# Kernel optimization log

Hardware: AMD Instinct MI355X
Metric: run time of the kernel (lower is better)

## Reference

```python
import jax, jax.numpy as jnp
import numpy as np


def setup_inputs() -> dict:
    key = jax.random.key(0)
    k1, k2, k3, k4, k5 = jax.random.split(key, 5)
    B, N, T, O, G = 32, 256, 1024, 1024, 8
    x = jax.random.normal(k1, (B, N, T), dtype=jnp.float32)
    y = jax.random.uniform(k2, (B, G), dtype=jnp.float32)  # genre mixture weights
    weight = jax.random.normal(k3, (G, O, T), dtype=jnp.float32) * (1.0 / np.sqrt(T))
    mask = jax.random.uniform(k4, (O, T), dtype=jnp.float32)
    bias = jax.random.normal(k5, (O,), dtype=jnp.float32)
    return {"x": x, "y": y, "weight": weight, "mask": mask, "bias": bias}


def reference(x, y, weight, mask, bias):
    # mask the shared weight bank: [G,O,T] * [1,O,T]
    masked_w = weight * mask[None, :, :]
    # per-sample genre-mixed weights: [B,G] x [G,O,T] -> [B,O,T]
    w_bot = jnp.einsum('bg,got->bot', y, masked_w)
    # batched masked linear: [B,N,T] x [B,O,T] -> [B,N,O], plus bias
    return jnp.einsum('bnt,bot->bno', x, w_bot) + bias
```

## Files before the change

kernel.cpp:

```cpp
#include <hip/hip_runtime.h>
#include <hip/hip_bf16.h>
#include <stdint.h>


#define B_ 32
#define N_ 256
#define T_ 1024
#define O_ 1024
#define G_ 8

#define WSTRIDE ((size_t)(O_ * T_ + 2048))

#define BM 128
#define BN 128
#define BK 64
#define BUFSZ (BM * BK)

typedef __attribute__((__ext_vector_type__(8)))  __bf16 bf16x8;
typedef __attribute__((__ext_vector_type__(16))) float  f32x16;

__device__ __forceinline__ unsigned short f2bf(float f) {
    union { float f; uint32_t u; } v; v.f = f;
    uint32_t u = v.u;
    uint32_t r = (u + 0x7fffu + ((u >> 16) & 1u)) >> 16;
    return (unsigned short)r;
}

__device__ __forceinline__ uint4 pack8(const float* a) {
    uint4 r;
    r.x = (uint32_t)f2bf(a[0]) | ((uint32_t)f2bf(a[1]) << 16);
    r.y = (uint32_t)f2bf(a[2]) | ((uint32_t)f2bf(a[3]) << 16);
    r.z = (uint32_t)f2bf(a[4]) | ((uint32_t)f2bf(a[5]) << 16);
    r.w = (uint32_t)f2bf(a[6]) | ((uint32_t)f2bf(a[7]) << 16);
    return r;
}

#define MIXB 1024
#define CVTB 1024

__global__ __launch_bounds__(256) void prep_kernel(
    const float* __restrict__ w,
    const float* __restrict__ mask,
    const float* __restrict__ y,
    const float* __restrict__ x,
    unsigned short* __restrict__ Wb,
    unsigned short* __restrict__ xb)
{
    const int tid = threadIdx.x;
    if (blockIdx.x < MIXB) {
        const int idx = blockIdx.x * 256 + tid;
        const int o   = idx >> 8;
        const int t   = (idx & 255) << 2;

        const float4 m4 = *(const float4*)(mask + (size_t)o * T_ + t);

        float wv[G_][4];
#pragma unroll
        for (int g = 0; g < G_; ++g) {
            const float4 a = *(const float4*)(w + ((size_t)g * O_ + o) * T_ + t);
            wv[g][0] = a.x * m4.x; wv[g][1] = a.y * m4.y;
            wv[g][2] = a.z * m4.z; wv[g][3] = a.w * m4.w;
        }
        unsigned short* dst = Wb + (size_t)o * T_ + t;
        const int bph = blockIdx.x & (B_ - 1);
#pragma unroll 4
        for (int bi = 0; bi < B_; ++bi) {
            const int b = (bi + bph) & (B_ - 1);
            const float4 y0 = *(const float4*)(y + b * G_);
            const float4 y1 = *(const float4*)(y + b * G_ + 4);
            const float yv[G_] = {y0.x, y0.y, y0.z, y0.w, y1.x, y1.y, y1.z, y1.w};
            float acc[4] = {};
#pragma unroll
            for (int g = 0; g < G_; ++g)
#pragma unroll
                for (int j = 0; j < 4; ++j)
                    acc[j] += yv[g] * wv[g][j];
            ushort4 pk;
            pk.x = f2bf(acc[0]); pk.y = f2bf(acc[1]);
            pk.z = f2bf(acc[2]); pk.w = f2bf(acc[3]);
            *(ushort4*)(dst + (size_t)b * WSTRIDE) = pk;
        }
    } else {
        const int i = (blockIdx.x - MIXB) * 256 + tid;
        const float4* x4 = (const float4*)x;
        uint4* o4 = (uint4*)xb;
#pragma unroll
        for (int j = 0; j < 4; ++j) {
            const size_t f4 = (size_t)j * 524288 + (size_t)i * 2;
            const float4 a = x4[f4];
            const float4 b = x4[f4 + 1];
            const float v[8] = {a.x, a.y, a.z, a.w, b.x, b.y, b.z, b.w};
            o4[(size_t)j * 262144 + i] = pack8(v);
        }
    }
}

__device__ __forceinline__ void load16_to_lds(const unsigned short* g, unsigned short* l) {
    __builtin_amdgcn_global_load_lds(
        (const __attribute__((address_space(1))) unsigned char*)g,
        (__attribute__((address_space(3))) unsigned char*)l,
        16, 0, 0);
}

__global__ __launch_bounds__(256, 2) void gemm_kernel(
    const unsigned short* __restrict__ xb,
    const unsigned short* __restrict__ Wb,
    const float* __restrict__ bias,
    float* __restrict__ out)
{
    __shared__ __align__(16) unsigned short lA[2 * BUFSZ];
    __shared__ __align__(16) unsigned short lB[2 * BUFSZ];

    const int tn = blockIdx.x;
    const int tm = blockIdx.y;
    const int b  = blockIdx.z;

    const int tid  = threadIdx.x;
    const int lane = tid & 63;
    const int wave = tid >> 6;
    const int wm   = (wave >> 1) * 64;
    const int wn   = (wave & 1) * 64;

    const unsigned short* Ab = xb + (size_t)b * N_ * T_ + (size_t)(tm * BM) * T_;
    const unsigned short* Bb = Wb + (size_t)b * WSTRIDE + (size_t)(tn * BN) * T_;

    const int srow   = tid >> 3;
    const int schunk = (tid & 7) ^ (srow & 7);
    const unsigned short* ga0 = Ab + (size_t)srow * T_ + schunk * 8;
    const unsigned short* gb0 = Bb + (size_t)srow * T_ + schunk * 8;

#define STAGE(buf, kt)                                                          \
    {                                                                           \
        unsigned short* lad = lA + (buf) * BUFSZ + tid * 8;                     \
        unsigned short* lbd = lB + (buf) * BUFSZ + tid * 8;                     \
        _Pragma("unroll")                                                       \
        for (int i_ = 0; i_ < 4; ++i_) {                                        \
            load16_to_lds(ga0 + (kt) + (size_t)(i_ * 32) * T_, lad + i_ * 2048);\
            load16_to_lds(gb0 + (kt) + (size_t)(i_ * 32) * T_, lbd + i_ * 2048);\
        }                                                                       \
    }

    f32x16 acc[2][2] = {};

    const int fr   = lane & 31;
    const int half = lane >> 5;
    const int sw   = fr & 7;

#define COMPUTE(buf)                                                            \
    {                                                                           \
        const unsigned short* la = lA + (buf) * BUFSZ;                          \
        const unsigned short* lb = lB + (buf) * BUFSZ;                          \
        _Pragma("unroll")                                                       \
        for (int ks = 0; ks < 4; ++ks) {                                        \
            const int cp = (((ks * 2 + half)) ^ sw) * 8;                        \
            bf16x8 afr[2], bfr[2];                                              \
            _Pragma("unroll")                                                   \
            for (int i_ = 0; i_ < 2; ++i_)                                      \
                afr[i_] = *(const bf16x8*)(la + (wm + i_ * 32 + fr) * BK + cp); \
            _Pragma("unroll")                                                   \
            for (int i_ = 0; i_ < 2; ++i_)                                      \
                bfr[i_] = *(const bf16x8*)(lb + (wn + i_ * 32 + fr) * BK + cp); \
            _Pragma("unroll")                                                   \
            for (int mi = 0; mi < 2; ++mi)                                      \
                _Pragma("unroll")                                               \
                for (int ni = 0; ni < 2; ++ni)                                  \
                    acc[mi][ni] = __builtin_amdgcn_mfma_f32_32x32x16_bf16(      \
                        afr[mi], bfr[ni], acc[mi][ni], 0, 0, 0);                \
        }                                                                       \
    }

    STAGE(0, 0)
    for (int kt = 0; kt < T_; kt += 2 * BK) {
        __syncthreads();
        STAGE(1, kt + BK)
        COMPUTE(0)
        __syncthreads();
        if (kt + 2 * BK < T_) STAGE(0, kt + 2 * BK)
        COMPUTE(1)
    }

    float* outb = out + (size_t)b * N_ * O_ + (size_t)(tm * BM) * O_ + (tn * BN);
    const int cn = lane & 31;
    const int rb = (lane >> 5) * 4;
#pragma unroll
    for (int ni = 0; ni < 2; ++ni) {
        const int col = wn + ni * 32 + cn;
        const float bv = bias[tn * BN + col];
#pragma unroll
        for (int mi = 0; mi < 2; ++mi) {
#pragma unroll
            for (int r = 0; r < 16; ++r) {
                const int row = wm + mi * 32 + rb + (r & 3) + 8 * (r >> 2);
                outb[(size_t)row * O_ + col] = acc[mi][ni][r] + bv;
            }
        }
    }
}

__global__ __launch_bounds__(256) void naive_kernel(
    const float* __restrict__ x, const float* __restrict__ y,
    const float* __restrict__ w, const float* __restrict__ mask,
    const float* __restrict__ bias, float* __restrict__ out)
{
    const int oc = blockIdx.x & 3;
    const int n  = (blockIdx.x >> 2) & (N_ - 1);
    const int b  = blockIdx.x >> 10;

    __shared__ float xs[T_];
    __shared__ float ys[G_];
    const float* xrow = x + ((size_t)b * N_ + n) * T_;
    for (int i = threadIdx.x; i < T_ / 4; i += 256)
        ((float4*)xs)[i] = ((const float4*)xrow)[i];
    if (threadIdx.x < G_) ys[threadIdx.x] = y[b * G_ + threadIdx.x];
    __syncthreads();

    const int o = oc * 256 + threadIdx.x;
    float acc = 0.f;
    for (int t = 0; t < T_; t += 4) {
        const float4 m4 = *(const float4*)(mask + (size_t)o * T_ + t);
        float4 s = {0.f, 0.f, 0.f, 0.f};
#pragma unroll
        for (int g = 0; g < G_; ++g) {
            const float4 w4 = *(const float4*)(w + ((size_t)g * O_ + o) * T_ + t);
            const float yv = ys[g];
            s.x += yv * w4.x; s.y += yv * w4.y; s.z += yv * w4.z; s.w += yv * w4.w;
        }
        acc += xs[t] * m4.x * s.x + xs[t + 1] * m4.y * s.y
             + xs[t + 2] * m4.z * s.z + xs[t + 3] * m4.w * s.w;
    }
    out[((size_t)b * N_ + n) * O_ + o] = acc + bias[o];
}

extern "C" void kernel_launch(void* const* d_in, const int* in_sizes, int n_in,
                              void* d_out, int out_size, void* d_ws, size_t ws_size,
                              hipStream_t stream) {
    const float* x    = (const float*)d_in[0];
    const float* y    = (const float*)d_in[1];
    const float* w    = (const float*)d_in[2];
    const float* mask = (const float*)d_in[3];
    const float* bias = (const float*)d_in[4];
    float* out = (float*)d_out;

    const size_t wb_bytes = (size_t)B_ * WSTRIDE * sizeof(unsigned short);
    const size_t xb_bytes = (size_t)B_ * N_ * T_ * sizeof(unsigned short);

    if (ws_size >= wb_bytes + xb_bytes) {
        unsigned short* Wb = (unsigned short*)d_ws;
        unsigned short* xb = (unsigned short*)((char*)d_ws + wb_bytes);
        prep_kernel<<<MIXB + CVTB, 256, 0, stream>>>(w, mask, y, x, Wb, xb);
        dim3 grid(O_ / BN, N_ / BM, B_);
        gemm_kernel<<<grid, 256, 0, stream>>>(xb, Wb, bias, out);
    } else {
        naive_kernel<<<B_ * N_ * (O_ / 256), 256, 0, stream>>>(x, y, w, mask, bias, out);
    }
}
```

Baseline: 159.6 us.

## Store mixed bf16 weights O-major with interleaved batches and stage y in LDS

The mixed-weight buffer changes from [B][O][T] with padded stride to [O][B][T], so each prep thread writes contiguous batch rows for one output row. Work is split into 4 batch-quarter blocks per output row instead of looping over all 32 batches. y is cached in shared memory, and the GEMM B-tile loads use the new row stride B*T. This aims to improve write locality and parallelism in prep, but GEMM B loads now stride by B*T between rows, which may hurt cache and TLB behaviour. It also drops the padding that was presumably there to avoid channel conflicts.

```diff
diff --git a/kernel.cpp b/kernel.cpp
--- a/kernel.cpp
+++ b/kernel.cpp
@@ -9,12 +9,12 @@
 #define O_ 1024
 #define G_ 8
 
-#define WSTRIDE ((size_t)(O_ * T_ + 2048))
-
 #define BM 128
 #define BN 128
 #define BK 64
 #define BUFSZ (BM * BK)
+
+#define BROW ((size_t)(B_ * T_))
 
 typedef __attribute__((__ext_vector_type__(8)))  __bf16 bf16x8;
 typedef __attribute__((__ext_vector_type__(16))) float  f32x16;
@@ -35,7 +35,7 @@
     return r;
 }
 
-#define MIXB 1024
+#define MIXB 4096
 #define CVTB 1024
 
 __global__ __launch_bounds__(256) void prep_kernel(
@@ -48,9 +48,13 @@
 {
     const int tid = threadIdx.x;
     if (blockIdx.x < MIXB) {
-        const int idx = blockIdx.x * 256 + tid;
-        const int o   = idx >> 8;
-        const int t   = (idx & 255) << 2;
+        __shared__ float ys[B_ * G_];
+        ys[tid] = y[tid];
+        __syncthreads();
+
+        const int bq  = blockIdx.x & 3;
+        const int o   = blockIdx.x >> 2;
+        const int t   = tid << 2;
 
         const float4 m4 = *(const float4*)(mask + (size_t)o * T_ + t);
 
@@ -61,13 +65,13 @@
             wv[g][0] = a.x * m4.x; wv[g][1] = a.y * m4.y;
             wv[g][2] = a.z * m4.z; wv[g][3] = a.w * m4.w;
         }
-        unsigned short* dst = Wb + (size_t)o * T_ + t;
-        const int bph = blockIdx.x & (B_ - 1);
-#pragma unroll 4
-        for (int bi = 0; bi < B_; ++bi) {
-            const int b = (bi + bph) & (B_ - 1);
-            const float4 y0 = *(const float4*)(y + b * G_);
-            const float4 y1 = *(const float4*)(y + b * G_ + 4);
+        unsigned short* dst = Wb + (size_t)o * BROW + t;
+        const int bph = (blockIdx.x >> 2) & 7;
+#pragma unroll
+        for (int bi = 0; bi < 8; ++bi) {
+            const int b = bq * 8 + ((bi + bph) & 7);
+            const float4 y0 = *(const float4*)(ys + b * G_);
+            const float4 y1 = *(const float4*)(ys + b * G_ + 4);
             const float yv[G_] = {y0.x, y0.y, y0.z, y0.w, y1.x, y1.y, y1.z, y1.w};
             float acc[4] = {};
 #pragma unroll
@@ -78,7 +82,7 @@
             ushort4 pk;
             pk.x = f2bf(acc[0]); pk.y = f2bf(acc[1]);
             pk.z = f2bf(acc[2]); pk.w = f2bf(acc[3]);
-            *(ushort4*)(dst + (size_t)b * WSTRIDE) = pk;
+            *(ushort4*)(dst + (size_t)b * T_) = pk;
         }
     } else {
         const int i = (blockIdx.x - MIXB) * 256 + tid;
@@ -122,12 +126,12 @@
     const int wn   = (wave & 1) * 64;
 
     const unsigned short* Ab = xb + (size_t)b * N_ * T_ + (size_t)(tm * BM) * T_;
-    const unsigned short* Bb = Wb + (size_t)b * WSTRIDE + (size_t)(tn * BN) * T_;
+    const unsigned short* Bb = Wb + (size_t)(tn * BN) * BROW + (size_t)b * T_;
 
     const int srow   = tid >> 3;
     const int schunk = (tid & 7) ^ (srow & 7);
     const unsigned short* ga0 = Ab + (size_t)srow * T_ + schunk * 8;
-    const unsigned short* gb0 = Bb + (size_t)srow * T_ + schunk * 8;
+    const unsigned short* gb0 = Bb + (size_t)srow * BROW + schunk * 8;
 
 #define STAGE(buf, kt)                                                          \
     {                                                                           \
@@ -136,7 +140,7 @@
         _Pragma("unroll")                                                       \
         for (int i_ = 0; i_ < 4; ++i_) {                                        \
             load16_to_lds(ga0 + (kt) + (size_t)(i_ * 32) * T_, lad + i_ * 2048);\
-            load16_to_lds(gb0 + (kt) + (size_t)(i_ * 32) * T_, lbd + i_ * 2048);\
+            load16_to_lds(gb0 + (kt) + (size_t)(i_ * 32) * BROW, lbd + i_ * 2048);\
         }                                                                       \
     }
 
@@ -241,7 +245,7 @@
     const float* bias = (const float*)d_in[4];
     float* out = (float*)d_out;
 
-    const size_t wb_bytes = (size_t)B_ * WSTRIDE * sizeof(unsigned short);
+    const size_t wb_bytes = (size_t)O_ * B_ * T_ * sizeof(unsigned short);
     const size_t xb_bytes = (size_t)B_ * N_ * T_ * sizeof(unsigned short);
 
     if (ws_size >= wb_bytes + xb_bytes) {
```

After: 175.1 us. +9.7%, slower.
